# Kernel optimization log

Hardware: AMD Instinct MI355X
Metric: run time of the kernel (lower is better)

Reference implementation:

```python
import jax, jax.numpy as jnp
import numpy as np

NUM_EMBEDDINGS = 4096
EMBEDDING_DIM = 64
COMMITMENT_COST = 0.25
DECAY = 0.99
EPSILON = 1e-05


def setup_inputs() -> dict:
    key = jax.random.key(0)
    k1, k2, k3, k4 = jax.random.split(key, 4)
    z = jax.random.normal(k1, (128, 24, 1536), dtype=jnp.float32)
    embedding = jax.random.normal(k2, (NUM_EMBEDDINGS, EMBEDDING_DIM), dtype=jnp.float32) * 0.05
    ema_cluster_size = jax.random.uniform(k3, (NUM_EMBEDDINGS,), dtype=jnp.float32)
    ema_w = jax.random.normal(k4, (NUM_EMBEDDINGS, EMBEDDING_DIM), dtype=jnp.float32) * 0.05
    return {"z": z, "embedding": embedding, "ema_cluster_size": ema_cluster_size, "ema_w": ema_w}


def reference(z, embedding, ema_cluster_size, ema_w):
    # VectorQuantizer.forward in training mode (EMA codebook update).
    K, d = embedding.shape
    B = z.shape[0]
    z_flat = z.reshape(-1, d)  # [N, d], N = B*576

    # Pairwise squared distances: ||z||^2 + ||e||^2 - 2 z e^T  -> [N, K]
    dist = (jnp.sum(z_flat * z_flat, axis=1, keepdims=True)
            + jnp.sum(embedding * embedding, axis=1)
            - 2.0 * (z_flat @ embedding.T))
    codes = jnp.argmin(dist, axis=1)  # [N]

    # EMA statistics (one-hot scatter expressed as segment sums)
    counts = jax.ops.segment_sum(jnp.ones_like(codes, dtype=z.dtype), codes, num_segments=K)
    new_cluster_size = DECAY * ema_cluster_size + (1.0 - DECAY) * counts
    dw = jax.ops.segment_sum(z_flat, codes, num_segments=K)  # [K, d]
    new_ema_w = DECAY * ema_w + (1.0 - DECAY) * dw

    n = jnp.sum(new_cluster_size)
    cluster_size = (new_cluster_size + EPSILON) / (n + K * EPSILON) * n
    new_embedding = new_ema_w / cluster_size[:, None]

    # Quantize with the UPDATED codebook (torch copies weights before embedding lookup)
    z_q = new_embedding[codes].reshape(z.shape)
    vq_loss = COMMITMENT_COST * jnp.mean((jax.lax.stop_gradient(z_q) - z) ** 2)
    z_q_st = z + jax.lax.stop_gradient(z_q - z)  # straight-through
    codes = codes.reshape(B, -1)  # [B, 576]
    return (vq_loss, z_q_st, codes, new_embedding, new_cluster_size, new_ema_w)
```

## Files before the change

### kernel.cpp

```cpp
#include <hip/hip_runtime.h>

constexpr int KC    = 4096;
constexpr int DIM   = 64;
constexpr int NROWS = 73728;
constexpr int NELEM = 4718592;
constexpr int RB    = 4096;
constexpr int RING  = 12;

typedef _Float16 f16x8 __attribute__((ext_vector_type(8)));
typedef float    f32x4 __attribute__((ext_vector_type(4)));

constexpr size_t OUT_LOSS  = 0;
constexpr size_t OUT_ZQ    = 1;
constexpr size_t OUT_CODES = 1 + (size_t)NELEM;
constexpr size_t OUT_EMB   = OUT_CODES + (size_t)NROWS;
constexpr size_t OUT_NCS   = OUT_EMB + (size_t)KC * DIM;
constexpr size_t OUT_NEW   = OUT_NCS + (size_t)KC;

constexpr size_t alignup(size_t x, size_t a) { return (x + a - 1) & ~(a - 1); }
constexpr size_t WS_CODES  = 0;
constexpr size_t WS_COUNTS = WS_CODES + sizeof(int) * (size_t)NROWS;
constexpr size_t WS_OFFS   = WS_COUNTS + sizeof(int) * (size_t)KC;
constexpr size_t WS_CURSOR = alignup(WS_OFFS + sizeof(int) * (KC + 1), 16);
constexpr size_t WS_SORTED = WS_CURSOR + sizeof(int) * (size_t)KC;
constexpr size_t WS_E2     = alignup(WS_SORTED + sizeof(int) * (size_t)NROWS, 64);
constexpr size_t WS_N      = WS_E2 + sizeof(float) * (size_t)KC;
constexpr size_t WS_LOSSD  = alignup(WS_N + sizeof(float), 8);
constexpr size_t WS_EMBPK  = alignup(WS_LOSSD + 8, 64);

__device__ __forceinline__ void gload16(const void* g, void* l) {
    __builtin_amdgcn_global_load_lds(
        (const __attribute__((address_space(1))) unsigned int*)g,
        (__attribute__((address_space(3))) unsigned int*)l, 16, 0, 0);
}

__global__ void k_prep(const float* __restrict__ emb, char* __restrict__ emb_pk,
                       float* __restrict__ e2s, int* __restrict__ counts) {
    if (threadIdx.x < 32) counts[blockIdx.x * 32 + threadIdx.x] = 0;
    int t = blockIdx.x * 256 + threadIdx.x;
    int c = t >> 3, q = t & 7;
    const float* ep = emb + (size_t)c * DIM + q * 8;
    f16x8 hv, lv;
    float s = 0.f;
    #pragma unroll
    for (int e = 0; e < 8; ++e) {
        float x = ep[e];
        _Float16 h = (_Float16)x;
        float r = x - (float)h;
        hv[e] = h;
        lv[e] = (_Float16)(r * 2048.0f);
        s = fmaf(x, x, s);
    }
    s += __shfl_xor(s, 1, 64);
    s += __shfl_xor(s, 2, 64);
    s += __shfl_xor(s, 4, 64);
    if (q == 0) e2s[c] = 1024.0f * s;
    int g = c >> 4, lc = c & 15;
    int h = q >> 2, lq = q & 3;
    int lane = lq * 16 + lc;
    char* base = emb_pk + (size_t)g * RB + lane * 16;
    *(f16x8*)(base + h * 1024)       = hv;
    *(f16x8*)(base + (2 + h) * 1024) = lv;
}

__global__ __launch_bounds__(192, 2) void k_argmin8(
        const float* __restrict__ z, const char* __restrict__ emb_pk,
        const float* __restrict__ e2s,
        int* __restrict__ codes_i, float* __restrict__ codes_f,
        int* __restrict__ counts) {
    __shared__ __align__(16) char lds[RING * RB + 16384];
    __shared__ int codebuf[3][48];
    constexpr int E2OFF = RING * RB;

    const int tid = threadIdx.x;
    const int l   = tid & 63;
    const int w   = tid >> 6;
    const int lc  = l & 15;
    const int lq  = l >> 4;
    const int waveRow = blockIdx.x * 144 + w * 48;

    f16x8 ah2k[3][2], ahr[3][2], al2k[3][2];
    #pragma unroll
    for (int rt = 0; rt < 3; ++rt)
        #pragma unroll
        for (int h = 0; h < 2; ++h) {
            const float* zp = z + (size_t)(waveRow + rt * 16 + lc) * DIM + h * 32 + lq * 8;
            float4 x0 = *(const float4*)zp;
            float4 x1 = *(const float4*)(zp + 4);
            float xs[8] = {x0.x, x0.y, x0.z, x0.w, x1.x, x1.y, x1.z, x1.w};
            #pragma unroll
            for (int e = 0; e < 8; ++e) {
                _Float16 hh = (_Float16)xs[e];
                float rr = xs[e] - (float)hh;
                ahr[rt][h][e]  = -hh;
                ah2k[rt][h][e] = (_Float16)(-2048.0f * (float)hh);
                al2k[rt][h][e] = -(_Float16)(rr * 2048.0f);
            }
        }

    float best[3][4];
    int   bestg[3][4];
    #pragma unroll
    for (int rt = 0; rt < 3; ++rt)
        #pragma unroll
        for (int j = 0; j < 4; ++j) { best[rt][j] = INFINITY; bestg[rt][j] = 0; }

#define STAGE(GS) {                                                         \
        int slot_ = (GS) % RING;                                            \
        int gsrc_ = (GS) < 256 ? (GS) : 255;                                \
        const char* gp_ = emb_pk + (size_t)gsrc_ * RB + (l << 4);           \
        char* lp_ = lds + slot_ * RB;                                       \
        gload16(gp_ + w * 1024, lp_ + w * 1024);                            \
        gload16(gp_ + 3072,     lp_ + 3072); }

#define LOADL(EV, B0, B1, B2, B3, G) {                                      \
        const char* p_ = lds + ((G) % RING) * RB + (l << 4);                \
        B0 = *(const f16x8*)(p_);                                           \
        B1 = *(const f16x8*)(p_ + 1024);                                    \
        B2 = *(const f16x8*)(p_ + 2048);                                    \
        B3 = *(const f16x8*)(p_ + 3072);                                    \
        EV = *(const float*)(lds + E2OFF + (((G) * 16 + lc) << 2)); }

#define COMP(B0, B1, B2, B3, EV, G) {                                             \
        f32x4 ci; ci[0] = EV; ci[1] = EV; ci[2] = EV; ci[3] = EV;                 \
        _Pragma("unroll")                                                         \
        for (int rt = 0; rt < 3; ++rt) {                                          \
            f32x4 acc = __builtin_amdgcn_mfma_f32_16x16x32_f16(ah2k[rt][0], B0, ci, 0, 0, 0); \
            acc = __builtin_amdgcn_mfma_f32_16x16x32_f16(ah2k[rt][1], B1, acc, 0, 0, 0);      \
            acc = __builtin_amdgcn_mfma_f32_16x16x32_f16(ahr[rt][0],  B2, acc, 0, 0, 0);      \
            acc = __builtin_amdgcn_mfma_f32_16x16x32_f16(ahr[rt][1],  B3, acc, 0, 0, 0);      \
            acc = __builtin_amdgcn_mfma_f32_16x16x32_f16(al2k[rt][0], B0, acc, 0, 0, 0);      \
            acc = __builtin_amdgcn_mfma_f32_16x16x32_f16(al2k[rt][1], B1, acc, 0, 0, 0);      \
            _Pragma("unroll")                                                     \
            for (int j = 0; j < 4; ++j) {                                         \
                if (acc[j] < best[rt][j]) { best[rt][j] = acc[j]; bestg[rt][j] = (G); } \
            }                                                                     \
        } }

    for (int s = w; s < 16; s += 3)
        gload16((const char*)e2s + s * 1024 + (l << 4), lds + E2OFF + s * 1024);
    for (int gs = 0; gs < 8; ++gs) STAGE(gs);
    asm volatile("s_waitcnt vmcnt(16)" ::: "memory");
    __builtin_amdgcn_s_barrier();
    __builtin_amdgcn_sched_barrier(0);

    {
        f16x8 A0, A1, A2, A3, B0, B1, B2, B3;
        float eA, eB;
        for (int t = 0; t < 256; t += 4) {
            asm volatile("s_waitcnt vmcnt(8)" ::: "memory");
            __builtin_amdgcn_s_barrier();
            __builtin_amdgcn_sched_barrier(0);
            LOADL(eA, A0, A1, A2, A3, t);
            LOADL(eB, B0, B1, B2, B3, t + 1);
            COMP(A0, A1, A2, A3, eA, t);
            LOADL(eA, A0, A1, A2, A3, t + 2);
            COMP(B0, B1, B2, B3, eB, t + 1);
            LOADL(eB, B0, B1, B2, B3, t + 3);
            COMP(A0, A1, A2, A3, eA, t + 2);
            COMP(B0, B1, B2, B3, eB, t + 3);
            STAGE(t + 8) STAGE(t + 9) STAGE(t + 10) STAGE(t + 11)
        }
    }
    asm volatile("s_waitcnt vmcnt(0)" ::: "memory");
    __builtin_amdgcn_sched_barrier(0);
#undef STAGE
#undef LOADL
#undef COMP

    #pragma unroll
    for (int rt = 0; rt < 3; ++rt)
        #pragma unroll
        for (int j = 0; j < 4; ++j) {
            float b = best[rt][j];
            int   k = bestg[rt][j] * 16 + lc;
            #pragma unroll
            for (int m = 1; m < 16; m <<= 1) {
                float obv = __shfl_xor(b, m, 64);
                int   okv = __shfl_xor(k, m, 64);
                if (obv < b || (obv == b && okv < k)) { b = obv; k = okv; }
            }
            if (lc == 0) codebuf[w][rt * 16 + lq * 4 + j] = k;
        }

    if (l < 48) {
        int code = codebuf[w][l];
        size_t rowg = (size_t)waveRow + l;
        codes_i[rowg] = code;
        codes_f[rowg] = (float)code;
        atomicAdd(&counts[code], 1);
    }
}

__global__ void k_scan(const int* __restrict__ counts,
                       int* __restrict__ offsets, int* __restrict__ cursor,
                       const float* __restrict__ ema_cs, float* __restrict__ ncs_out,
                       float* __restrict__ n_out, double* __restrict__ lossp) {
    __shared__ int   part[256];
    __shared__ float fpart[256];
    int tid = threadIdx.x;
    if (tid == 0) *lossp = 0.0;
    int base = tid * 16;
    int loc[16];
    int s = 0;
    float fs = 0.f;
    #pragma unroll
    for (int j = 0; j < 16; ++j) {
        int cnt = counts[base + j];
        loc[j] = s; s += cnt;
        float v = 0.99f * ema_cs[base + j] + 0.01f * (float)cnt;
        ncs_out[base + j] = v;
        fs += v;
    }
    part[tid] = s;
    fpart[tid] = fs;
    __syncthreads();
    for (int off = 1; off < 256; off <<= 1) {
        int v = (tid >= off) ? part[tid - off] : 0;
        __syncthreads();
        part[tid] += v;
        __syncthreads();
    }
    int excl = part[tid] - s;
    #pragma unroll
    for (int j = 0; j < 16; ++j) {
        int o = excl + loc[j];
        offsets[base + j] = o;
        cursor[base + j]  = o;
    }
    if (tid == 255) offsets[KC] = excl + s;
    for (int m = 128; m > 0; m >>= 1) {
        if (tid < m) fpart[tid] += fpart[tid + m];
        __syncthreads();
    }
    if (tid == 0) n_out[0] = fpart[0];
}

__global__ void k_scatteridx(const int* __restrict__ codes_i,
                             int* __restrict__ cursor, int* __restrict__ sorted_rows) {
    int r = blockIdx.x * 256 + threadIdx.x;
    if (r < NROWS) {
        int c = codes_i[r];
        int p = atomicAdd(&cursor[c], 1);
        sorted_rows[p] = r;
    }
}

__global__ __launch_bounds__(64) void k_dwsum(
        const float* __restrict__ z, const int* __restrict__ offsets,
        const int* __restrict__ sorted_rows, const float* __restrict__ ema_w,
        const float* __restrict__ ncs, const float* __restrict__ nptr,
        float* __restrict__ new_ema_w_out, float* __restrict__ new_emb_out) {
    int k = blockIdx.x, tid = threadIdx.x;
    int beg = offsets[k], end = offsets[k + 1];
    float a0 = 0.f, a1 = 0.f, a2 = 0.f, a3 = 0.f;
    int i = beg;
    for (; i + 3 < end; i += 4) {
        int r0 = sorted_rows[i], r1 = sorted_rows[i + 1];
        int r2 = sorted_rows[i + 2], r3 = sorted_rows[i + 3];
        a0 += z[(size_t)r0 * DIM + tid];
        a1 += z[(size_t)r1 * DIM + tid];
        a2 += z[(size_t)r2 * DIM + tid];
        a3 += z[(size_t)r3 * DIM + tid];
    }
    for (; i < end; ++i) a0 += z[(size_t)sorted_rows[i] * DIM + tid];
    float dwv = (a0 + a1) + (a2 + a3);
    size_t idx = (size_t)k * DIM + tid;
    float n = nptr[0];
    float nw = 0.99f * ema_w[idx] + 0.01f * dwv;
    float cs = (ncs[k] + 1e-5f) / (n + 4096.0f * 1e-5f) * n;
    new_ema_w_out[idx] = nw;
    new_emb_out[idx] = nw / cs;
}

__global__ __launch_bounds__(256) void k_quant(
        const float* __restrict__ z, const float* __restrict__ new_emb,
        const int* __restrict__ codes, float* __restrict__ zq_out,
        double* __restrict__ loss_acc) {
    __shared__ double red[256];
    const int nvec = NELEM / 4;
    int t = blockIdx.x * 256 + threadIdx.x;
    int stride = gridDim.x * 256;
    double ls = 0.0;
    for (int v = t; v < nvec; v += stride) {
        int e0 = v * 4;
        int n  = e0 >> 6;
        int d0 = e0 & 63;
        int code = codes[n];
        float4 zq = *(const float4*)&new_emb[(size_t)code * DIM + d0];
        float4 zv = *(const float4*)&z[e0];
        float dx = zq.x - zv.x, dy = zq.y - zv.y, dz = zq.z - zv.z, dw4 = zq.w - zv.w;
        float4 o;
        o.x = zv.x + dx; o.y = zv.y + dy; o.z = zv.z + dz; o.w = zv.w + dw4;
        *(float4*)&zq_out[e0] = o;
        ls += (double)(dx * dx) + (double)(dy * dy) + (double)(dz * dz) + (double)(dw4 * dw4);
    }
    red[threadIdx.x] = ls;
    __syncthreads();
    for (int m = 128; m > 0; m >>= 1) {
        if (threadIdx.x < m) red[threadIdx.x] += red[threadIdx.x + m];
        __syncthreads();
    }
    if (threadIdx.x == 0) atomicAdd(loss_acc, red[0]);
}

__global__ void k_loss(const double* __restrict__ loss_acc, float* __restrict__ out0) {
    out0[0] = (float)(0.25 * (loss_acc[0] / (double)NELEM));
}

extern "C" void kernel_launch(void* const* d_in, const int* in_sizes, int n_in,
                              void* d_out, int out_size, void* d_ws, size_t ws_size,
                              hipStream_t stream) {
    const float* z      = (const float*)d_in[0];
    const float* emb    = (const float*)d_in[1];
    const float* ema_cs = (const float*)d_in[2];
    const float* ema_w  = (const float*)d_in[3];
    float* out = (float*)d_out;
    char*  ws  = (char*)d_ws;

    int*    codes_i = (int*)(ws + WS_CODES);
    int*    counts  = (int*)(ws + WS_COUNTS);
    int*    offsets = (int*)(ws + WS_OFFS);
    int*    cursor  = (int*)(ws + WS_CURSOR);
    int*    sorted  = (int*)(ws + WS_SORTED);
    float*  e2s     = (float*)(ws + WS_E2);
    float*  nptr    = (float*)(ws + WS_N);
    double* lossp   = (double*)(ws + WS_LOSSD);
    char*   emb_pk  = ws + WS_EMBPK;

    k_prep<<<(KC * 8) / 256, 256, 0, stream>>>(emb, emb_pk, e2s, counts);
    k_argmin8<<<NROWS / 144, 192, 0, stream>>>(z, emb_pk, e2s, codes_i,
                                               out + OUT_CODES, counts);
    k_scan<<<1, 256, 0, stream>>>(counts, offsets, cursor, ema_cs,
                                  out + OUT_NCS, nptr, lossp);
    k_scatteridx<<<(NROWS + 255) / 256, 256, 0, stream>>>(codes_i, cursor, sorted);
    k_dwsum<<<KC, 64, 0, stream>>>(z, offsets, sorted, ema_w,
                                   out + OUT_NCS, nptr, out + OUT_NEW, out + OUT_EMB);
    k_quant<<<1152, 256, 0, stream>>>(z, out + OUT_EMB, codes_i,
                                      out + OUT_ZQ, lossp);
    k_loss<<<1, 1, 0, stream>>>(lossp, out + OUT_LOSS);
}
```

Before: 177.8 us.

## Restructure argmin kernel to two waves with 8-slot ring and explicit LDS waits

The argmin kernel now uses 2 waves (96 rows) per block instead of 3, shrinks the LDS ring from 12 to 8 slots, and issues the next four codebook stages at the start of each iteration. LDS reads become inline ds_read_b128 assembly with explicit lgkmcnt waits so MFMA work can start before all fragments land. The goal is less LDS per block for higher occupancy and finer overlap of shared-memory reads with compute. In exchange it waits for vmcnt(0) every iteration, which shortens the global prefetch distance and may expose load latency.

Result: slower. 181.7 us (+2.2%).

```diff
diff --git a/kernel.cpp b/kernel.cpp
--- a/kernel.cpp
+++ b/kernel.cpp
@@ -5,7 +5,7 @@
 constexpr int NROWS = 73728;
 constexpr int NELEM = 4718592;
 constexpr int RB    = 4096;
-constexpr int RING  = 12;
+constexpr int RING  = 8;
 
 typedef _Float16 f16x8 __attribute__((ext_vector_type(8)));
 typedef float    f32x4 __attribute__((ext_vector_type(4)));
@@ -63,13 +63,13 @@
     *(f16x8*)(base + (2 + h) * 1024) = lv;
 }
 
-__global__ __launch_bounds__(192, 2) void k_argmin8(
+__global__ __launch_bounds__(128, 2) void k_argmin9(
         const float* __restrict__ z, const char* __restrict__ emb_pk,
         const float* __restrict__ e2s,
         int* __restrict__ codes_i, float* __restrict__ codes_f,
         int* __restrict__ counts) {
     __shared__ __align__(16) char lds[RING * RB + 16384];
-    __shared__ int codebuf[3][48];
+    __shared__ int codebuf[2][48];
     constexpr int E2OFF = RING * RB;
 
     const int tid = threadIdx.x;
@@ -77,7 +77,8 @@
     const int w   = tid >> 6;
     const int lc  = l & 15;
     const int lq  = l >> 4;
-    const int waveRow = blockIdx.x * 144 + w * 48;
+    const int waveRow = blockIdx.x * 96 + w * 48;
+    const unsigned ldsbase = (unsigned)(unsigned long long)(void*)lds;
 
     f16x8 ah2k[3][2], ahr[3][2], al2k[3][2];
     #pragma unroll
@@ -106,20 +107,24 @@
         for (int j = 0; j < 4; ++j) { best[rt][j] = INFINITY; bestg[rt][j] = 0; }
 
 #define STAGE(GS) {                                                         \
-        int slot_ = (GS) % RING;                                            \
         int gsrc_ = (GS) < 256 ? (GS) : 255;                                \
         const char* gp_ = emb_pk + (size_t)gsrc_ * RB + (l << 4);           \
-        char* lp_ = lds + slot_ * RB;                                       \
-        gload16(gp_ + w * 1024, lp_ + w * 1024);                            \
-        gload16(gp_ + 3072,     lp_ + 3072); }
+        char* lp_ = lds + ((GS) & 7) * RB;                                  \
+        gload16(gp_ + w * 1024,        lp_ + w * 1024);                     \
+        gload16(gp_ + (w + 2) * 1024,  lp_ + (w + 2) * 1024); }
 
 #define LOADL(EV, B0, B1, B2, B3, G) {                                      \
-        const char* p_ = lds + ((G) % RING) * RB + (l << 4);                \
-        B0 = *(const f16x8*)(p_);                                           \
-        B1 = *(const f16x8*)(p_ + 1024);                                    \
-        B2 = *(const f16x8*)(p_ + 2048);                                    \
-        B3 = *(const f16x8*)(p_ + 3072);                                    \
-        EV = *(const float*)(lds + E2OFF + (((G) * 16 + lc) << 2)); }
+        unsigned a_ = ldsbase + (unsigned)(((G) & 7) * RB) + (l << 4);      \
+        asm volatile("ds_read_b128 %0, %1"             : "=v"(B0) : "v"(a_)); \
+        asm volatile("ds_read_b128 %0, %1 offset:1024" : "=v"(B1) : "v"(a_)); \
+        asm volatile("ds_read_b128 %0, %1 offset:2048" : "=v"(B2) : "v"(a_)); \
+        asm volatile("ds_read_b128 %0, %1 offset:3072" : "=v"(B3) : "v"(a_)); \
+        unsigned e_ = ldsbase + E2OFF + (unsigned)((((G) * 16 + lc)) << 2); \
+        asm volatile("ds_read_b32 %0, %1"              : "=v"(EV) : "v"(e_)); }
+
+#define WAITL(N)                                                            \
+        asm volatile("s_waitcnt lgkmcnt(" #N ")" ::: "memory");             \
+        __builtin_amdgcn_sched_barrier(0);
 
 #define COMP(B0, B1, B2, B3, EV, G) {                                             \
         f32x4 ci; ci[0] = EV; ci[1] = EV; ci[2] = EV; ci[3] = EV;                 \
@@ -137,35 +142,35 @@
             }                                                                     \
         } }
 
-    for (int s = w; s < 16; s += 3)
+    for (int s = w; s < 16; s += 2)
         gload16((const char*)e2s + s * 1024 + (l << 4), lds + E2OFF + s * 1024);
-    for (int gs = 0; gs < 8; ++gs) STAGE(gs);
-    asm volatile("s_waitcnt vmcnt(16)" ::: "memory");
-    __builtin_amdgcn_s_barrier();
+    STAGE(0) STAGE(1) STAGE(2) STAGE(3)
     __builtin_amdgcn_sched_barrier(0);
 
     {
         f16x8 A0, A1, A2, A3, B0, B1, B2, B3;
         float eA, eB;
+        #pragma unroll 1
         for (int t = 0; t < 256; t += 4) {
-            asm volatile("s_waitcnt vmcnt(8)" ::: "memory");
+            asm volatile("s_waitcnt vmcnt(0)" ::: "memory");
             __builtin_amdgcn_s_barrier();
             __builtin_amdgcn_sched_barrier(0);
-            LOADL(eA, A0, A1, A2, A3, t);
-            LOADL(eB, B0, B1, B2, B3, t + 1);
-            COMP(A0, A1, A2, A3, eA, t);
-            LOADL(eA, A0, A1, A2, A3, t + 2);
-            COMP(B0, B1, B2, B3, eB, t + 1);
-            LOADL(eB, B0, B1, B2, B3, t + 3);
-            COMP(A0, A1, A2, A3, eA, t + 2);
-            COMP(B0, B1, B2, B3, eB, t + 3);
-            STAGE(t + 8) STAGE(t + 9) STAGE(t + 10) STAGE(t + 11)
+            STAGE(t + 4) STAGE(t + 5) STAGE(t + 6) STAGE(t + 7)
+            LOADL(eA, A0, A1, A2, A3, t)
+            LOADL(eB, B0, B1, B2, B3, t + 1)
+            WAITL(5)  COMP(A0, A1, A2, A3, eA, t)
+            LOADL(eA, A0, A1, A2, A3, t + 2)
+            WAITL(5)  COMP(B0, B1, B2, B3, eB, t + 1)
+            LOADL(eB, B0, B1, B2, B3, t + 3)
+            WAITL(5)  COMP(A0, A1, A2, A3, eA, t + 2)
+            WAITL(0)  COMP(B0, B1, B2, B3, eB, t + 3)
         }
     }
     asm volatile("s_waitcnt vmcnt(0)" ::: "memory");
     __builtin_amdgcn_sched_barrier(0);
 #undef STAGE
 #undef LOADL
+#undef WAITL
 #undef COMP
 
     #pragma unroll
@@ -329,8 +334,8 @@
     char*   emb_pk  = ws + WS_EMBPK;
 
     k_prep<<<(KC * 8) / 256, 256, 0, stream>>>(emb, emb_pk, e2s, counts);
-    k_argmin8<<<NROWS / 144, 192, 0, stream>>>(z, emb_pk, e2s, codes_i,
-                                               out + OUT_CODES, counts);
+    k_argmin9<<<NROWS / 96, 128, 0, stream>>>(z, emb_pk, e2s, codes_i,
+                                              out + OUT_CODES, counts);
     k_scan<<<1, 256, 0, stream>>>(counts, offsets, cursor, ema_cs,
                                   out + OUT_NCS, nptr, lossp);
     k_scatteridx<<<(NROWS + 255) / 256, 256, 0, stream>>>(codes_i, cursor, sorted);
```
